# Kernel optimization log

Measured on AMD Instinct MI355X. Metric: run time of the kernel, lower is better.

The kernel has to match this reference:

```python
import jax, jax.numpy as jnp
import numpy as np

HEADS = 8

def setup_inputs() -> dict:
    key = jax.random.key(0)
    ks = jax.random.split(key, 7)
    B, C, H, W = 8, 640, 64, 64
    L, CD = 77, 768
    return {
        "hidden_states": jax.random.normal(ks[0], (B, C, H, W), jnp.float32),
        "encoder_hidden_states": jax.random.normal(ks[1], (B, L, CD), jnp.float32),
        "Wq": jax.random.normal(ks[2], (C, C), jnp.float32) * 0.02,
        "Wk": jax.random.normal(ks[3], (CD, C), jnp.float32) * 0.02,
        "Wv": jax.random.normal(ks[4], (CD, C), jnp.float32) * 0.02,
        "Wo": jax.random.normal(ks[5], (C, C), jnp.float32) * 0.02,
        "bo": jnp.zeros((C,), jnp.float32),
    }

def reference(hidden_states, encoder_hidden_states, Wq, Wk, Wv, Wo, bo):
    B, C, H, W = hidden_states.shape
    N = H * W
    dh = C // HEADS
    scale = 1.0 / jnp.sqrt(jnp.asarray(dh, hidden_states.dtype))
    # (B, C, H, W) -> (B, N, C)
    x = hidden_states.reshape(B, C, N).transpose(0, 2, 1)
    q = (x @ Wq).reshape(B, N, HEADS, dh)
    k = (encoder_hidden_states @ Wk).reshape(B, -1, HEADS, dh)
    v = (encoder_hidden_states @ Wv).reshape(B, -1, HEADS, dh)
    # scores: (B, HEADS, N, L) -- full attention_probs materialized as in the original
    scores = jnp.einsum("bnhd,blhd->bhnl", q, k) * scale
    probs = jax.nn.softmax(scores, axis=-1)
    # saliency capture: mean over heads then over k tokens -> (B, 1, H, W)
    saliency = probs.mean(axis=1).mean(axis=-1).reshape(B, 1, H, W)
    out = jnp.einsum("bhnl,blhd->bnhd", probs, v).reshape(B, N, C)
    out = out @ Wo + bo
    out = out.transpose(0, 2, 1).reshape(B, C, H, W)
    return out, saliency
```

## Files before the change

### kernel.cpp

```cpp
#include <hip/hip_runtime.h>

typedef unsigned short u16;
typedef __bf16 bf16x8 __attribute__((ext_vector_type(8)));
typedef float f32x4 __attribute__((ext_vector_type(4)));
typedef unsigned short u16x8 __attribute__((ext_vector_type(8)));
typedef unsigned short u16x4 __attribute__((ext_vector_type(4)));

#define NB 8
#define NC 640
#define NN 4096
#define NL 77
#define NCD 768
#define NH 8
#define NDH 80

__device__ __forceinline__ u16 f2bf(float f) {
  unsigned u = __builtin_bit_cast(unsigned, f);
  u += 0x7fffu + ((u >> 16) & 1u);
  return (u16)(u >> 16);
}

__device__ __forceinline__ f32x4 mfma16(bf16x8 a, bf16x8 b, f32x4 c) {
  return __builtin_amdgcn_mfma_f32_16x16x32_bf16(a, b, c, 0, 0, 0);
}

__device__ __forceinline__ void gload_lds16(const void* g, void* l) {
  __builtin_amdgcn_global_load_lds(
      (const __attribute__((address_space(1))) void*)g,
      (__attribute__((address_space(3))) void*)l, 16, 0, 0);
}

__global__ __launch_bounds__(256) void k_prep(const float* __restrict__ ehs,
                                              const float* __restrict__ Wq,
                                              const float* __restrict__ Wk,
                                              const float* __restrict__ Wv,
                                              const float* __restrict__ Wo,
                                              u16* __restrict__ wqt,
                                              u16* __restrict__ wot,
                                              u16* __restrict__ kbf,
                                              u16* __restrict__ vtbf,
                                              float* __restrict__ sal) {
  __shared__ __align__(16) char smem[37888];
  const int bid = blockIdx.x;
  const int t = threadIdx.x;

  if (bid < 800) {
    float(*tls)[33] = (float(*)[33])smem;
    const int which = bid / 400;
    const int rem = bid % 400;
    const float* in = which ? Wo : Wq;
    u16* outp = which ? wot : wqt;
    const float scale = which ? 1.0f : 0.11180339887498949f;
    const int n0 = (rem % 20) * 32, k0 = (rem / 20) * 32;
    const int r = t >> 3, c4 = (t & 7) * 4;
    float4 v = *(const float4*)(in + (size_t)(k0 + r) * NC + n0 + c4);
    tls[r][c4 + 0] = v.x; tls[r][c4 + 1] = v.y; tls[r][c4 + 2] = v.z; tls[r][c4 + 3] = v.w;
    __syncthreads();
    u16x4 o;
#pragma unroll
    for (int e = 0; e < 4; ++e) o[e] = f2bf(tls[c4 + e][r] * scale);
    *(u16x4*)(outp + (size_t)(n0 + r) * NC + k0 + c4) = o;
    return;
  }
  if (bid < 1760) {
    const int i = bid - 800;
    const int l = i % 96, cg = i / 96;
    if (l >= NL) {
      if (t < 64) {
        int c = cg * 64 + t;
        int h = c / NDH, d = c % NDH;
#pragma unroll
        for (int b = 0; b < NB; ++b)
          vtbf[(((size_t)(b * NH + h)) * NDH + d) * 96 + l] = 0;
      }
      return;
    }
    float(*es)[NCD] = (float(*)[NCD])smem;
    float(*comb)[64][17] = (float(*)[64][17])(smem + 24576);
#pragma unroll
    for (int j = 0; j < 6; ++j) {
      int idx = (t + j * 256) * 4;
      int b = idx / NCD, k = idx % NCD;
      *(float4*)&es[b][k] = *(const float4*)(ehs + ((size_t)(b * NL + l)) * NCD + k);
    }
    __syncthreads();
    const int col = t & 63, kq = t >> 6;
    const int c = cg * 64 + col;
    float ak[NB], av[NB];
#pragma unroll
    for (int b = 0; b < NB; ++b) { ak[b] = 0.f; av[b] = 0.f; }
    const int kbeg = kq * 192, kend = kbeg + 192;
#pragma unroll 4
    for (int k = kbeg; k < kend; ++k) {
      float wk = Wk[(size_t)k * NC + c];
      float wv = Wv[(size_t)k * NC + c];
#pragma unroll
      for (int b = 0; b < NB; ++b) {
        ak[b] = fmaf(es[b][k], wk, ak[b]);
        av[b] = fmaf(es[b][k], wv, av[b]);
      }
    }
    if (kq) {
#pragma unroll
      for (int b = 0; b < NB; ++b) {
        comb[kq - 1][col][b] = ak[b];
        comb[kq - 1][col][8 + b] = av[b];
      }
    }
    __syncthreads();
    if (kq == 0) {
#pragma unroll
      for (int b = 0; b < NB; ++b) {
#pragma unroll
        for (int q = 0; q < 3; ++q) {
          ak[b] += comb[q][col][b];
          av[b] += comb[q][col][8 + b];
        }
      }
      const int h = c / NDH, d = c % NDH;
#pragma unroll
      for (int b = 0; b < NB; ++b) {
        kbf[(((size_t)(b * NH + h)) * 80 + l) * 80 + d] = f2bf(ak[b]);
        vtbf[(((size_t)(b * NH + h)) * NDH + d) * 96 + l] = f2bf(av[b]);
      }
    }
    return;
  }
  {
    int i = (bid - 1760) * 256 + t;
    if (i < NB * NN) sal[i] = 1.0f / 77.0f;
  }
}

__global__ __launch_bounds__(256, 3) void k_gemm_q(const float* __restrict__ hs,
                                                   const u16* __restrict__ Bw,
                                                   u16* __restrict__ outb) {
  __shared__ __align__(16) u16 sB[128 * 64];
  const int bid = blockIdx.x;
  const int logical = (bid & 7) * 160 + (bid >> 3);
  const int cb = logical % 5, rb = logical / 5;
  const int r0 = rb * 128, c0 = cb * 128;
  const int t = threadIdx.x;
  const int w = t >> 6, lane = t & 63;
  const int wm = w >> 1, wn = w & 1;
  const int fr = lane & 15, g = lane >> 4;
  const int lr = lane >> 3, ls = lane & 7;
  const int sslot = ls ^ lr;
  const int b = r0 >> 12, n0 = r0 & 4095;
  const int nbase = n0 + wm * 64 + fr;

  f32x4 acc[4][4];
  f32x4 z4 = {0.f, 0.f, 0.f, 0.f};
#pragma unroll
  for (int i = 0; i < 4; ++i)
#pragma unroll
    for (int j = 0; j < 4; ++j) acc[i][j] = z4;

  for (int ks = 0; ks < 10; ++ks) {
    const int k0 = ks * 64;
#pragma unroll
    for (int p = 0; p < 4; ++p) {
      int q = w * 4 + p;
      int row = q * 8 + lr;
      gload_lds16(Bw + (size_t)(c0 + row) * NC + k0 + sslot * 8, sB + q * 512);
    }
    bf16x8 af[4][2];
#pragma unroll
    for (int kk = 0; kk < 2; ++kk) {
      const float* hp = hs + (((size_t)(b * NC + k0 + kk * 32 + g * 8)) << 12) + nbase;
#pragma unroll
      for (int mt = 0; mt < 4; ++mt) {
        float tmp[8];
#pragma unroll
        for (int j = 0; j < 8; ++j) tmp[j] = hp[((size_t)j << 12) + mt * 16];
        u16x8 pk;
#pragma unroll
        for (int j = 0; j < 8; ++j) pk[j] = f2bf(tmp[j]);
        af[mt][kk] = __builtin_bit_cast(bf16x8, pk);
      }
    }
    asm volatile("s_waitcnt vmcnt(0)" ::: "memory");
    __syncthreads();
#pragma unroll
    for (int kk = 0; kk < 2; ++kk) {
      bf16x8 bfr[4];
#pragma unroll
      for (int nt = 0; nt < 4; ++nt) {
        int row = wn * 64 + nt * 16 + fr;
        bfr[nt] = *(const bf16x8*)((const char*)sB + row * 128 +
                                   ((kk * 64 + g * 16) ^ ((row & 7) << 4)));
      }
#pragma unroll
      for (int mt = 0; mt < 4; ++mt)
#pragma unroll
        for (int nt = 0; nt < 4; ++nt)
          acc[mt][nt] = mfma16(bfr[nt], af[mt][kk], acc[mt][nt]);
    }
    __syncthreads();
  }
#pragma unroll
  for (int mt = 0; mt < 4; ++mt) {
    int n = n0 + wm * 64 + mt * 16 + fr;
#pragma unroll
    for (int nt = 0; nt < 4; ++nt) {
      int cbs = c0 + wn * 64 + nt * 16 + g * 4;
      u16x4 o;
#pragma unroll
      for (int r2 = 0; r2 < 4; ++r2) o[r2] = f2bf(acc[mt][nt][r2]);
      *(u16x4*)(outb + ((size_t)(b * NN + n)) * NC + cbs) = o;
    }
  }
}

__global__ __launch_bounds__(256) void k_gemm_o(const u16* __restrict__ A,
                                                const u16* __restrict__ Bw,
                                                const float* __restrict__ bias,
                                                float* __restrict__ outf) {
  __shared__ __align__(16) u16 sA[128 * 64];
  __shared__ __align__(16) u16 sB[128 * 64];
  const int bid = blockIdx.x;
  const int logical = (bid & 7) * 160 + (bid >> 3);
  const int cb = logical % 5, rb = logical / 5;
  const int r0 = rb * 128, c0 = cb * 128;
  const int t = threadIdx.x;
  const int w = t >> 6, lane = t & 63;
  const int wm = w >> 1, wn = w & 1;
  const int fr = lane & 15, g = lane >> 4;
  const int lr = lane >> 3, ls = lane & 7;
  const int sslot = ls ^ lr;

  f32x4 acc[4][4];
  f32x4 z4 = {0.f, 0.f, 0.f, 0.f};
#pragma unroll
  for (int i = 0; i < 4; ++i)
#pragma unroll
    for (int j = 0; j < 4; ++j) acc[i][j] = z4;

  for (int ks = 0; ks < 10; ++ks) {
    const int k0 = ks * 64;
#pragma unroll
    for (int p = 0; p < 4; ++p) {
      int q = w * 4 + p;
      int row = q * 8 + lr;
      gload_lds16(A + (size_t)(r0 + row) * NC + k0 + sslot * 8, sA + q * 512);
      gload_lds16(Bw + (size_t)(c0 + row) * NC + k0 + sslot * 8, sB + q * 512);
    }
    asm volatile("s_waitcnt vmcnt(0)" ::: "memory");
    __syncthreads();
#pragma unroll
    for (int kk = 0; kk < 2; ++kk) {
      bf16x8 af[4], bfr[4];
#pragma unroll
      for (int mt = 0; mt < 4; ++mt) {
        int row = wm * 64 + mt * 16 + fr;
        af[mt] = *(const bf16x8*)((const char*)sA + row * 128 +
                                  ((kk * 64 + g * 16) ^ ((row & 7) << 4)));
      }
#pragma unroll
      for (int nt = 0; nt < 4; ++nt) {
        int row = wn * 64 + nt * 16 + fr;
        bfr[nt] = *(const bf16x8*)((const char*)sB + row * 128 +
                                   ((kk * 64 + g * 16) ^ ((row & 7) << 4)));
      }
#pragma unroll
      for (int mt = 0; mt < 4; ++mt)
#pragma unroll
        for (int nt = 0; nt < 4; ++nt)
          acc[mt][nt] = mfma16(af[mt], bfr[nt], acc[mt][nt]);
    }
    __syncthreads();
  }
  const int b = r0 >> 12, n0 = r0 & 4095;
#pragma unroll
  for (int mt = 0; mt < 4; ++mt) {
    int n = n0 + wm * 64 + mt * 16 + g * 4;
#pragma unroll
    for (int nt = 0; nt < 4; ++nt) {
      int c = c0 + wn * 64 + nt * 16 + fr;
      float bv = bias[c];
      f32x4 o;
#pragma unroll
      for (int r2 = 0; r2 < 4; ++r2) o[r2] = acc[mt][nt][r2] + bv;
      *(f32x4*)(outf + (((size_t)(b * NC + c)) << 12) + n) = o;
    }
  }
}

__global__ __launch_bounds__(256) void k_attn(const u16* __restrict__ qbf,
                                              const u16* __restrict__ kbf,
                                              const u16* __restrict__ vtbf,
                                              u16* __restrict__ obf) {
  __shared__ __align__(16) u16 sP[4][16][104];
  const int bid = blockIdx.x;
  const int n0 = (bid & 63) * 64, h = (bid >> 6) & 7, b = bid >> 9;
  const int t = threadIdx.x, w = t >> 6, lane = t & 63;
  const int fr = lane & 15, g = lane >> 4;

  const size_t qrow = ((size_t)(b * NN + n0 + w * 16 + fr)) * NC + h * NDH;
  bf16x8 qf[3];
#pragma unroll
  for (int kk = 0; kk < 3; ++kk) {
    int d0 = kk * 32 + g * 8;
    bf16x8 v = {};
    if (d0 < NDH) v = *(const bf16x8*)(qbf + qrow + d0);
    qf[kk] = v;
  }
  const size_t kbase = ((size_t)(b * NH + h)) * (80 * 80);
  f32x4 s[5];
  f32x4 z4 = {0.f, 0.f, 0.f, 0.f};
#pragma unroll
  for (int nt = 0; nt < 5; ++nt) s[nt] = z4;
#pragma unroll
  for (int nt = 0; nt < 5; ++nt) {
    const u16* krow = kbf + kbase + (size_t)(nt * 16 + fr) * 80;
#pragma unroll
    for (int kk = 0; kk < 3; ++kk) {
      int d0 = kk * 32 + g * 8;
      bf16x8 kv = {};
      if (d0 < NDH) kv = *(const bf16x8*)(krow + d0);
      s[nt] = mfma16(kv, qf[kk], s[nt]);
    }
  }
  const size_t vbase = ((size_t)(b * NH + h)) * (80 * 96);
  bf16x8 vf[5][3];
#pragma unroll
  for (int nt = 0; nt < 5; ++nt)
#pragma unroll
    for (int kk = 0; kk < 3; ++kk)
      vf[nt][kk] = *(const bf16x8*)(vtbf + vbase + (size_t)(nt * 16 + fr) * 96 +
                                    kk * 32 + g * 8);
  float sum = 0.f;
#pragma unroll
  for (int nt = 0; nt < 5; ++nt)
#pragma unroll
    for (int r = 0; r < 4; ++r) {
      int l = nt * 16 + g * 4 + r;
      float ev = (l < NL) ? __expf(s[nt][r]) : 0.f;
      s[nt][r] = ev;
      sum += ev;
    }
  sum += __shfl_xor(sum, 16);
  sum += __shfl_xor(sum, 32);
  float inv = 1.0f / sum;
#pragma unroll
  for (int nt = 0; nt < 5; ++nt) {
    u16x4 o;
#pragma unroll
    for (int r = 0; r < 4; ++r) o[r] = f2bf(s[nt][r] * inv);
    *(u16x4*)&sP[w][fr][nt * 16 + g * 4] = o;
  }
  __syncthreads();
  bf16x8 ap[3];
#pragma unroll
  for (int kk = 0; kk < 3; ++kk) {
    int l0 = kk * 32 + g * 8;
    bf16x8 v = {};
    if (l0 < 80) v = *(const bf16x8*)&sP[w][fr][l0];
    ap[kk] = v;
  }
  f32x4 o[5];
#pragma unroll
  for (int nt = 0; nt < 5; ++nt) o[nt] = z4;
#pragma unroll
  for (int nt = 0; nt < 5; ++nt)
#pragma unroll
    for (int kk = 0; kk < 3; ++kk)
      o[nt] = mfma16(ap[kk], vf[nt][kk], o[nt]);
#pragma unroll
  for (int nt = 0; nt < 5; ++nt)
#pragma unroll
    for (int r = 0; r < 4; ++r)
      obf[((size_t)(b * NN + n0 + w * 16 + g * 4 + r)) * NC + h * NDH + nt * 16 + fr] =
          f2bf(o[nt][r]);
}

extern "C" void kernel_launch(void* const* d_in, const int* in_sizes, int n_in,
                              void* d_out, int out_size, void* d_ws, size_t ws_size,
                              hipStream_t stream) {
  const float* hs  = (const float*)d_in[0];
  const float* ehs = (const float*)d_in[1];
  const float* Wq  = (const float*)d_in[2];
  const float* Wk  = (const float*)d_in[3];
  const float* Wv  = (const float*)d_in[4];
  const float* Wo  = (const float*)d_in[5];
  const float* bo  = (const float*)d_in[6];
  float* out = (float*)d_out;
  float* sal = out + (size_t)NB * NC * NN;

  u16* ws16 = (u16*)d_ws;
  const size_t xn = (size_t)NB * NN * NC;
  u16* obf = ws16;
  u16* qbf = ws16 + xn;
  u16* wqt = qbf + xn;
  u16* wot = wqt + (size_t)NC * NC;
  u16* kbf = wot + (size_t)NC * NC;
  u16* vtbf = kbf + (size_t)NB * NH * 80 * 80;

  k_prep<<<1888, 256, 0, stream>>>(ehs, Wq, Wk, Wv, Wo,
                                   wqt, wot, kbf, vtbf, sal);
  k_gemm_q<<<1280, 256, 0, stream>>>(hs, wqt, qbf);
  k_attn<<<NB * NH * 64, 256, 0, stream>>>(qbf, kbf, vtbf, obf);
  k_gemm_o<<<1280, 256, 0, stream>>>(obf, wot, bo, out);
}
```

Before: 176.2 us.

## Pre-transpose hidden states to bf16 and fuse KV projection with Q GEMM

The prep kernel now converts and transposes the fp32 NCHW hidden states into a bf16 row-major (B,N,C) buffer. The Q GEMM then loads both operands via direct global-to-LDS copies instead of strided fp32 gathers with per-element conversion. The K/V projection blocks move into the same launch as the Q GEMM so the two overlap. This trades an extra full write and read of the activation tensor for coalesced, conversion-free GEMM loads, and it reuses the output workspace to hold the transposed input.

```diff
diff --git a/kernel.cpp b/kernel.cpp
--- a/kernel.cpp
+++ b/kernel.cpp
@@ -30,17 +30,14 @@
       (__attribute__((address_space(3))) void*)l, 16, 0, 0);
 }
 
-__global__ __launch_bounds__(256) void k_prep(const float* __restrict__ ehs,
+__global__ __launch_bounds__(256) void k_prep(const float* __restrict__ hs,
                                               const float* __restrict__ Wq,
-                                              const float* __restrict__ Wk,
-                                              const float* __restrict__ Wv,
                                               const float* __restrict__ Wo,
+                                              u16* __restrict__ xbf,
                                               u16* __restrict__ wqt,
                                               u16* __restrict__ wot,
-                                              u16* __restrict__ kbf,
-                                              u16* __restrict__ vtbf,
                                               float* __restrict__ sal) {
-  __shared__ __align__(16) char smem[37888];
+  __shared__ __align__(16) char smem[17664];
   const int bid = blockIdx.x;
   const int t = threadIdx.x;
 
@@ -62,9 +59,51 @@
     *(u16x4*)(outp + (size_t)(n0 + r) * NC + k0 + c4) = o;
     return;
   }
-  if (bid < 1760) {
+  if (bid < 5920) {
+    float(*tls)[69] = (float(*)[69])smem;
     const int i = bid - 800;
-    const int l = i % 96, cg = i / 96;
+    const int n0 = (i % 64) * 64;
+    const int c0 = ((i / 64) % 10) * 64;
+    const int b = i / 640;
+    const int rr = t >> 4;
+    const int cc = (t & 15) * 4;
+#pragma unroll
+    for (int p = 0; p < 4; ++p) {
+      int c = p * 16 + rr;
+      float4 v = *(const float4*)(hs + ((size_t)(b * NC + c0 + c) << 12) + n0 + cc);
+      *(float4*)&tls[c][cc] = v;
+    }
+    __syncthreads();
+#pragma unroll
+    for (int p = 0; p < 4; ++p) {
+      int n = p * 16 + rr;
+      u16x4 o;
+#pragma unroll
+      for (int e = 0; e < 4; ++e) o[e] = f2bf(tls[cc + e][n]);
+      *(u16x4*)(xbf + ((size_t)(b * NN + n0 + n)) * NC + c0 + cc) = o;
+    }
+    return;
+  }
+  {
+    int i = (bid - 5920) * 256 + t;
+    if (i < NB * NN) sal[i] = 1.0f / 77.0f;
+  }
+}
+
+__global__ __launch_bounds__(256) void k_kvg0(const float* __restrict__ ehs,
+                                              const float* __restrict__ Wk,
+                                              const float* __restrict__ Wv,
+                                              u16* __restrict__ kbf,
+                                              u16* __restrict__ vtbf,
+                                              const u16* __restrict__ A,
+                                              const u16* __restrict__ Bw,
+                                              u16* __restrict__ outb) {
+  __shared__ __align__(16) char smem[32768];
+  const int bid = blockIdx.x;
+  const int t = threadIdx.x;
+
+  if (bid < 960) {
+    const int l = bid % 96, cg = bid / 96;
     if (l >= NL) {
       if (t < 64) {
         int c = cg * 64 + t;
@@ -76,7 +115,7 @@
       return;
     }
     float(*es)[NCD] = (float(*)[NCD])smem;
-    float(*comb)[64][17] = (float(*)[64][17])(smem + 24576);
+    float(*comb)[64][17] = (float(*)[64][17])smem;
 #pragma unroll
     for (int j = 0; j < 6; ++j) {
       int idx = (t + j * 256) * 4;
@@ -100,6 +139,7 @@
         av[b] = fmaf(es[b][k], wv, av[b]);
       }
     }
+    __syncthreads();
     if (kq) {
 #pragma unroll
       for (int b = 0; b < NB; ++b) {
@@ -126,28 +166,18 @@
     }
     return;
   }
-  {
-    int i = (bid - 1760) * 256 + t;
-    if (i < NB * NN) sal[i] = 1.0f / 77.0f;
-  }
-}
-
-__global__ __launch_bounds__(256, 3) void k_gemm_q(const float* __restrict__ hs,
-                                                   const u16* __restrict__ Bw,
-                                                   u16* __restrict__ outb) {
-  __shared__ __align__(16) u16 sB[128 * 64];
-  const int bid = blockIdx.x;
-  const int logical = (bid & 7) * 160 + (bid >> 3);
+
+  u16* sA = (u16*)smem;
+  u16* sB = (u16*)(smem + 16384);
+  const int bid2 = bid - 960;
+  const int logical = (bid2 & 7) * 160 + (bid2 >> 3);
   const int cb = logical % 5, rb = logical / 5;
   const int r0 = rb * 128, c0 = cb * 128;
-  const int t = threadIdx.x;
   const int w = t >> 6, lane = t & 63;
   const int wm = w >> 1, wn = w & 1;
   const int fr = lane & 15, g = lane >> 4;
   const int lr = lane >> 3, ls = lane & 7;
   const int sslot = ls ^ lr;
-  const int b = r0 >> 12, n0 = r0 & 4095;
-  const int nbase = n0 + wm * 64 + fr;
 
   f32x4 acc[4][4];
   f32x4 z4 = {0.f, 0.f, 0.f, 0.f};
@@ -162,28 +192,20 @@
     for (int p = 0; p < 4; ++p) {
       int q = w * 4 + p;
       int row = q * 8 + lr;
+      gload_lds16(A + (size_t)(r0 + row) * NC + k0 + sslot * 8, sA + q * 512);
       gload_lds16(Bw + (size_t)(c0 + row) * NC + k0 + sslot * 8, sB + q * 512);
     }
-    bf16x8 af[4][2];
+    asm volatile("s_waitcnt vmcnt(0)" ::: "memory");
+    __syncthreads();
 #pragma unroll
     for (int kk = 0; kk < 2; ++kk) {
-      const float* hp = hs + (((size_t)(b * NC + k0 + kk * 32 + g * 8)) << 12) + nbase;
+      bf16x8 af[4], bfr[4];
 #pragma unroll
       for (int mt = 0; mt < 4; ++mt) {
-        float tmp[8];
-#pragma unroll
-        for (int j = 0; j < 8; ++j) tmp[j] = hp[((size_t)j << 12) + mt * 16];
-        u16x8 pk;
-#pragma unroll
-        for (int j = 0; j < 8; ++j) pk[j] = f2bf(tmp[j]);
-        af[mt][kk] = __builtin_bit_cast(bf16x8, pk);
-      }
-    }
-    asm volatile("s_waitcnt vmcnt(0)" ::: "memory");
-    __syncthreads();
-#pragma unroll
-    for (int kk = 0; kk < 2; ++kk) {
-      bf16x8 bfr[4];
+        int row = wm * 64 + mt * 16 + fr;
+        af[mt] = *(const bf16x8*)((const char*)sA + row * 128 +
+                                  ((kk * 64 + g * 16) ^ ((row & 7) << 4)));
+      }
 #pragma unroll
       for (int nt = 0; nt < 4; ++nt) {
         int row = wn * 64 + nt * 16 + fr;
@@ -194,10 +216,11 @@
       for (int mt = 0; mt < 4; ++mt)
 #pragma unroll
         for (int nt = 0; nt < 4; ++nt)
-          acc[mt][nt] = mfma16(bfr[nt], af[mt][kk], acc[mt][nt]);
-    }
-    __syncthreads();
-  }
+          acc[mt][nt] = mfma16(bfr[nt], af[mt], acc[mt][nt]);
+    }
+    __syncthreads();
+  }
+  const int b = r0 >> 12, n0 = r0 & 4095;
 #pragma unroll
   for (int mt = 0; mt < 4; ++mt) {
     int n = n0 + wm * 64 + mt * 16 + fr;
@@ -389,16 +412,16 @@
 
   u16* ws16 = (u16*)d_ws;
   const size_t xn = (size_t)NB * NN * NC;
-  u16* obf = ws16;
+  u16* xbf = ws16;
   u16* qbf = ws16 + xn;
   u16* wqt = qbf + xn;
   u16* wot = wqt + (size_t)NC * NC;
   u16* kbf = wot + (size_t)NC * NC;
   u16* vtbf = kbf + (size_t)NB * NH * 80 * 80;
-
-  k_prep<<<1888, 256, 0, stream>>>(ehs, Wq, Wk, Wv, Wo,
-                                   wqt, wot, kbf, vtbf, sal);
-  k_gemm_q<<<1280, 256, 0, stream>>>(hs, wqt, qbf);
+  u16* obf = xbf;
+
+  k_prep<<<6048, 256, 0, stream>>>(hs, Wq, Wo, xbf, wqt, wot, sal);
+  k_kvg0<<<2240, 256, 0, stream>>>(ehs, Wk, Wv, kbf, vtbf, xbf, wqt, qbf);
   k_attn<<<NB * NH * 64, 256, 0, stream>>>(qbf, kbf, vtbf, obf);
   k_gemm_o<<<1280, 256, 0, stream>>>(obf, wot, bo, out);
 }
```

New measurement: 164.9 us. -6.4%, faster.
